# Kernel tuning notes

Measured on AMD Instinct MI355X. Metric: run time of the kernel, lower is better.

The kernel has to match this reference:

```python
import jax, jax.numpy as jnp
import numpy as np

N = 50000      # nodes
E = 800000     # edges
IN_DIM = 256
D = 32         # out_dim per head
H = 8          # num_heads
NEG_SLOPE = 0.01  # torch F.leaky_relu default


def setup_inputs() -> dict:
    key = jax.random.key(0)
    k1, k2, k3, k4, k5 = jax.random.split(key, 5)
    h = jax.random.normal(k1, (N, IN_DIM), dtype=jnp.float32)
    W = jax.random.normal(k2, (H, IN_DIM, D), dtype=jnp.float32) * 0.05
    attn_w = jax.random.normal(k3, (H, 2 * D), dtype=jnp.float32) * 0.05
    src = jax.random.randint(k4, (E,), 0, N, dtype=jnp.int64)
    dst = jax.random.randint(k5, (E,), 0, N, dtype=jnp.int64)
    return {"h": h, "W": W, "attn_w": attn_w, "src": src, "dst": dst}


def reference(h, W, attn_w, src, dst):
    # per-head linear projection: z[n,h,d]
    z = jnp.einsum('ni,hid->nhd', h, W)
    # attn_fc(concat(z_src, z_dst)) = z_src @ a_l + z_dst @ a_r
    a_l, a_r = attn_w[:, :D], attn_w[:, D:]
    el = jnp.einsum('nhd,hd->nh', z, a_l)  # [N,H]
    er = jnp.einsum('nhd,hd->nh', z, a_r)  # [N,H]
    e = jax.nn.leaky_relu(el[src] + er[dst], NEG_SLOPE)  # [E,H]
    # segment softmax over incoming edges of each destination node
    m = jax.ops.segment_max(e, dst, num_segments=N)      # [N,H]
    m = jnp.where(jnp.isfinite(m), m, 0.0)               # nodes w/ no in-edges
    num = jnp.exp(e - m[dst])                            # [E,H]
    den = jax.ops.segment_sum(num, dst, num_segments=N)  # [N,H]
    den_e = den[dst]
    alpha = num / jnp.where(den_e > 0, den_e, 1.0)       # [E,H]
    # weighted scatter-sum of source features
    msg = alpha[:, :, None] * z[src]                     # [E,H,D]
    hout = jax.ops.segment_sum(msg, dst, num_segments=N) # [N,H,D]
    # merge='cat': concat head outputs along feature dim
    return hout.reshape(N, H * D)
```

## Files before the change

### kernel.cpp

```cpp
#include <hip/hip_runtime.h>
#include <math.h>

#define NN 50000
#define EE 800000
#define INDIM 256
#define DD 32
#define HH 8
#define CC 256
#define NEG 0.01f
#define NREP 8
#define NSCAN 49
#define PREP_GRID 1024
#define PREP_STRIDE (PREP_GRID * 256)

typedef __attribute__((ext_vector_type(8))) short bf16x8;
typedef __attribute__((ext_vector_type(4))) float f32x4;

__device__ __forceinline__ unsigned short f32_to_bf16_rne(float f) {
  unsigned u = __float_as_uint(f);
  u += 0x7fffu + ((u >> 16) & 1u);
  return (unsigned short)(u >> 16);
}

__global__ __launch_bounds__(256) void k_prep(const unsigned* __restrict__ sraw,
                                              const unsigned* __restrict__ draw,
                                              int* __restrict__ counts8,
                                              unsigned short* __restrict__ s16,
                                              unsigned short* __restrict__ d16,
                                              unsigned short* __restrict__ slot16,
                                              const float* __restrict__ W,
                                              unsigned short* __restrict__ WbT) {
  __shared__ int sflag;
  if (threadIdx.x == 0) sflag = 0;
  __syncthreads();
  const int gt = blockIdx.x * 256 + threadIdx.x;
  unsigned v = 0;
#pragma unroll
  for (int i = 0; i < 4; ++i) {
    int e = (gt * 4 + i) % (EE / 2);
    v |= sraw[2 * e + 1] | draw[2 * e + 1];
  }
  if (v) atomicOr(&sflag, 1);
  __syncthreads();
  const int is32 = sflag;

  const int rep = blockIdx.x & (NREP - 1);
  int* __restrict__ mycounts = counts8 + rep * NN;

  for (int e = gt; e < EE; e += PREP_STRIDE) {
    int sv, dv;
    if (is32) {
      sv = ((const int*)sraw)[e];
      dv = ((const int*)draw)[e];
    } else {
      sv = (int)((const long long*)sraw)[e];
      dv = (int)((const long long*)draw)[e];
    }
    s16[e] = (unsigned short)sv;
    d16[e] = (unsigned short)dv;
    slot16[e] = (unsigned short)atomicAdd(&mycounts[dv], 1);
  }

  if (gt < INDIM * CC) {
    int n = gt >> 8, k = gt & 255;
    int hh = n >> 5, d = n & 31;
    WbT[gt] = f32_to_bf16_rne(W[(size_t)hh * 8192 + k * 32 + d]);
  }
}

__global__ __launch_bounds__(512) void k_gemm(const float* __restrict__ h,
                                              const unsigned short* __restrict__ WbT,
                                              const float* __restrict__ attn_w,
                                              signed char* __restrict__ z8,
                                              float* __restrict__ elsc,
                                              float* __restrict__ er) {
  __shared__ short sA[64 * 256];
  const int t = threadIdx.x;
  const int l = t & 63;
  const int w = t >> 6;
  const int row0 = blockIdx.x * 64;

#pragma unroll
  for (int i = 0; i < 4; ++i) {
    int q = i * 512 + t;
    int row = q >> 5, c = q & 31;
    int grow = row0 + row; if (grow >= NN) grow = NN - 1;
    const float* src = &h[(size_t)grow * 256 + c * 8];
    float4 f0 = *reinterpret_cast<const float4*>(src);
    float4 f1 = *reinterpret_cast<const float4*>(src + 4);
    bf16x8 vv;
    vv[0] = (short)f32_to_bf16_rne(f0.x); vv[1] = (short)f32_to_bf16_rne(f0.y);
    vv[2] = (short)f32_to_bf16_rne(f0.z); vv[3] = (short)f32_to_bf16_rne(f0.w);
    vv[4] = (short)f32_to_bf16_rne(f1.x); vv[5] = (short)f32_to_bf16_rne(f1.y);
    vv[6] = (short)f32_to_bf16_rne(f1.z); vv[7] = (short)f32_to_bf16_rne(f1.w);
    int sc = c ^ (row & 7);
    *reinterpret_cast<bf16x8*>(&sA[row * 256 + sc * 8]) = vv;
  }

  bf16x8 bf[2][8];
  {
    const int n = w * 32 + (l & 15);
    const int kb = (l >> 4) * 8;
#pragma unroll
    for (int c = 0; c < 2; ++c)
#pragma unroll
      for (int kk = 0; kk < 8; ++kk)
        bf[c][kk] = *reinterpret_cast<const bf16x8*>(
            &WbT[(size_t)(n + c * 16) * 256 + kk * 32 + kb]);
  }

  f32x4 acc[4][2];
#pragma unroll
  for (int m = 0; m < 4; ++m)
#pragma unroll
    for (int c = 0; c < 2; ++c) acc[m][c] = (f32x4){0.f, 0.f, 0.f, 0.f};

  __syncthreads();

#pragma unroll
  for (int kk = 0; kk < 8; ++kk) {
    bf16x8 af[4];
#pragma unroll
    for (int m = 0; m < 4; ++m) {
      int row = m * 16 + (l & 15);
      int chunk = kk * 4 + (l >> 4);
      int sc = chunk ^ (row & 7);
      af[m] = *reinterpret_cast<const bf16x8*>(&sA[row * 256 + sc * 8]);
    }
#pragma unroll
    for (int m = 0; m < 4; ++m)
#pragma unroll
      for (int c = 0; c < 2; ++c)
        acc[m][c] = __builtin_amdgcn_mfma_f32_16x16x32_bf16(bf[c][kk], af[m], acc[m][c], 0, 0, 0);
  }

  float alc[2][4], arc[2][4];
#pragma unroll
  for (int c = 0; c < 2; ++c)
#pragma unroll
    for (int r = 0; r < 4; ++r) {
      int d = c * 16 + ((l >> 4) << 2) + r;
      alc[c][r] = attn_w[w * 64 + d];
      arc[c][r] = attn_w[w * 64 + 32 + d];
    }

#pragma unroll
  for (int m = 0; m < 4; ++m) {
    int node = row0 + m * 16 + (l & 15);
    float pl = 0.f, pr = 0.f, pm = 0.f;
#pragma unroll
    for (int c = 0; c < 2; ++c)
#pragma unroll
      for (int r = 0; r < 4; ++r) {
        float a = acc[m][c][r];
        pl += a * alc[c][r];
        pr += a * arc[c][r];
        pm = fmaxf(pm, fabsf(a));
      }
    pl += __shfl_xor(pl, 16); pl += __shfl_xor(pl, 32);
    pr += __shfl_xor(pr, 16); pr += __shfl_xor(pr, 32);
    pm = fmaxf(pm, __shfl_xor(pm, 16)); pm = fmaxf(pm, __shfl_xor(pm, 32));
    const float rcp = (pm > 0.f) ? (127.f / pm) : 0.f;

    if (node < NN) {
#pragma unroll
      for (int c = 0; c < 2; ++c) {
        unsigned wq = 0;
#pragma unroll
        for (int r = 0; r < 4; ++r) {
          int q = __float2int_rn(acc[m][c][r] * rcp);
          wq |= ((unsigned)(q & 255)) << (8 * r);
        }
        *reinterpret_cast<unsigned*>(
            &z8[(size_t)node * CC + w * 32 + c * 16 + ((l >> 4) << 2)]) = wq;
      }
      if ((l >> 4) == 0) {
        elsc[(size_t)node * 16 + w] = pl;
        elsc[(size_t)node * 16 + 8 + w] = pm * (1.f / 127.f);
        er[(size_t)node * HH + w] = pr;
      }
    }
  }
}

__global__ __launch_bounds__(1024) void k_scan(const int* __restrict__ counts8,
                                               int* __restrict__ row_start,
                                               int* __restrict__ partial,
                                               unsigned char* __restrict__ offs8) {
  __shared__ int s[1024];
  const int tid = threadIdx.x;
  const int i = blockIdx.x * 1024 + tid;
  int deg = 0;
  if (i < NN) {
    unsigned pack0 = 0, pack1 = 0;
    int run = 0;
#pragma unroll
    for (int r = 0; r < NREP; ++r) {
      int c = counts8[r * NN + i];
      if (r < 4) pack0 |= (unsigned)run << (8 * r);
      else       pack1 |= (unsigned)run << (8 * (r - 4));
      run += c;
    }
    deg = run;
    uint2 pk; pk.x = pack0; pk.y = pack1;
    *reinterpret_cast<uint2*>(&offs8[(size_t)i * 8]) = pk;
  }
  s[tid] = deg;
  __syncthreads();
  for (int off = 1; off < 1024; off <<= 1) {
    int tv = (tid >= off) ? s[tid - off] : 0;
    __syncthreads();
    s[tid] += tv;
    __syncthreads();
  }
  if (i < NN) row_start[i] = s[tid] - deg;
  if (tid == 1023) partial[blockIdx.x] = s[1023];
}

__device__ __forceinline__ void block_base_scan(const int* __restrict__ partial,
                                                int* __restrict__ sbase) {
  if (threadIdx.x < 64) {
    int l = threadIdx.x;
    int x = (l < NSCAN) ? partial[l] : 0;
    int orig = x;
#pragma unroll
    for (int off = 1; off < 64; off <<= 1) {
      int y = __shfl_up(x, off);
      if (l >= off) x += y;
    }
    sbase[l] = x - orig;
  }
  __syncthreads();
}

__global__ __launch_bounds__(256) void k_scatter(const unsigned short* __restrict__ s16,
                                                 const unsigned short* __restrict__ d16,
                                                 const unsigned short* __restrict__ slot16,
                                                 const unsigned char* __restrict__ offs8,
                                                 const int* __restrict__ row_start,
                                                 const int* __restrict__ partial,
                                                 unsigned short* __restrict__ csr16) {
  __shared__ int sbase[64];
  block_base_scan(partial, sbase);
  int stride = gridDim.x * blockDim.x;
  for (int e = blockIdx.x * blockDim.x + threadIdx.x; e < EE; e += stride) {
    int dn = (int)d16[e];
    int rep = ((e & (PREP_STRIDE - 1)) >> 8) & (NREP - 1);
    int pos = row_start[dn] + sbase[dn >> 10] + (int)offs8[dn * 8 + rep] + (int)slot16[e];
    csr16[pos] = s16[e];
  }
}

#define AGG_WAVES 8192
__global__ __launch_bounds__(256) void k_agg(const signed char* __restrict__ z8,
                                             const float* __restrict__ elsc,
                                             const float* __restrict__ er,
                                             const int* __restrict__ row_start,
                                             const int* __restrict__ partial,
                                             const unsigned short* __restrict__ csr16,
                                             float* __restrict__ out) {
  __shared__ int sbase[64];
  block_base_scan(partial, sbase);

  const int gw = blockIdx.x * 4 + (threadIdx.x >> 6);
  const int l = threadIdx.x & 63;
  const int head = l >> 3;

  for (int n = gw; n < NN; n += AGG_WAVES) {
    const int beg = row_start[n] + sbase[n >> 10];
    const int end = (n == NN - 1) ? EE : (row_start[n + 1] + sbase[(n + 1) >> 10]);
    const float ern = er[(size_t)n * HH + head];

    float den = 0.f;
    float a0 = 0.f, a1 = 0.f, a2 = 0.f, a3 = 0.f;
#pragma unroll 4
    for (int p = beg; p < end; ++p) {
      int s = (int)csr16[p];
      float v = elsc[(size_t)s * 16 + head] + ern;
      v = (v > 0.f) ? v : v * NEG;
      float wgt = __expf(v);
      float sc = elsc[(size_t)s * 16 + 8 + head];
      unsigned wq = *reinterpret_cast<const unsigned*>(&z8[(size_t)s * CC + 4 * l]);
      den += wgt;
      float ws = wgt * sc;
      a0 += ws * (float)(int)(signed char)(wq & 255);
      a1 += ws * (float)(int)(signed char)((wq >> 8) & 255);
      a2 += ws * (float)(int)(signed char)((wq >> 16) & 255);
      a3 += ws * (float)(int)(signed char)(wq >> 24);
    }
    const float rd = (end > beg) ? (1.f / den) : 0.f;
    float4 o;
    o.x = a0 * rd; o.y = a1 * rd; o.z = a2 * rd; o.w = a3 * rd;
    *reinterpret_cast<float4*>(&out[(size_t)n * CC + 4 * l]) = o;
  }
}

extern "C" void kernel_launch(void* const* d_in, const int* in_sizes, int n_in,
                              void* d_out, int out_size, void* d_ws, size_t ws_size,
                              hipStream_t stream) {
  const float* h      = (const float*)d_in[0];
  const float* W      = (const float*)d_in[1];
  const float* attn_w = (const float*)d_in[2];
  const void*  src_raw = d_in[3];
  const void*  dst_raw = d_in[4];
  float* out = (float*)d_out;

  char* ws = (char*)d_ws;
  size_t off = 0;
  signed char* z8     = (signed char*)(ws + off); off += (size_t)NN * CC;
  unsigned short* WbT = (unsigned short*)(ws + off); off += (size_t)INDIM * CC * 2;
  float* elsc = (float*)(ws + off); off += (size_t)NN * 16 * 4;
  float* er   = (float*)(ws + off); off += (size_t)NN * HH * 4;
  int* counts8 = (int*)(ws + off); off += (size_t)NREP * NN * 4;
  int* row_start = (int*)(ws + off); off += (size_t)NN * 4;
  int* partial   = (int*)(ws + off); off += 256;
  unsigned char* offs8 = (unsigned char*)(ws + off); off += (size_t)NN * 8;
  unsigned short* s16    = (unsigned short*)(ws + off); off += (size_t)EE * 2;
  unsigned short* d16    = (unsigned short*)(ws + off); off += (size_t)EE * 2;
  unsigned short* slot16 = (unsigned short*)(ws + off); off += (size_t)EE * 2;
  unsigned short* csr16  = (unsigned short*)(ws + off); off += (size_t)EE * 2;

  hipMemsetAsync(counts8, 0, (size_t)NREP * NN * 4, stream);

  k_prep<<<PREP_GRID, 256, 0, stream>>>((const unsigned*)src_raw, (const unsigned*)dst_raw,
                                        counts8, s16, d16, slot16, W, WbT);

  k_gemm<<<(NN + 63) / 64, 512, 0, stream>>>(h, WbT, attn_w, z8, elsc, er);

  k_scan<<<NSCAN, 1024, 0, stream>>>(counts8, row_start, partial, offs8);

  k_scatter<<<2048, 256, 0, stream>>>(s16, d16, slot16, offs8, row_start, partial, csr16);

  k_agg<<<AGG_WAVES / 4, 256, 0, stream>>>(z8, elsc, er, row_start, partial, csr16, out);
}
```

Measured before the change: 146.6 us.

## Interleave two destination nodes per wave and pack el/scale as float2

The aggregation kernel now processes two destination nodes per wave, interleaving their edge loops over the common length so two independent gather chains are in flight. Tail loops finish the longer node. The per-node attention logit and quantization scale are stored interleaved as float2, so one 8-byte load replaces two scattered 4-byte loads. This raises memory-level parallelism for the latency-bound gathers, at the cost of more registers and possible imbalance between the paired nodes.

```diff
diff --git a/kernel.cpp b/kernel.cpp
--- a/kernel.cpp
+++ b/kernel.cpp
@@ -72,7 +72,7 @@
                                               const unsigned short* __restrict__ WbT,
                                               const float* __restrict__ attn_w,
                                               signed char* __restrict__ z8,
-                                              float* __restrict__ elsc,
+                                              float2* __restrict__ elsc,
                                               float* __restrict__ er) {
   __shared__ short sA[64 * 256];
   const int t = threadIdx.x;
@@ -175,8 +175,8 @@
             &z8[(size_t)node * CC + w * 32 + c * 16 + ((l >> 4) << 2)]) = wq;
       }
       if ((l >> 4) == 0) {
-        elsc[(size_t)node * 16 + w] = pl;
-        elsc[(size_t)node * 16 + 8 + w] = pm * (1.f / 127.f);
+        float2 e2; e2.x = pl; e2.y = pm * (1.f / 127.f);
+        elsc[(size_t)node * 8 + w] = e2;
         er[(size_t)node * HH + w] = pr;
       }
     }
@@ -252,8 +252,8 @@
 }
 
 #define AGG_WAVES 8192
-__global__ __launch_bounds__(256) void k_agg(const signed char* __restrict__ z8,
-                                             const float* __restrict__ elsc,
+__global__ __launch_bounds__(256) void k_agg(const unsigned* __restrict__ z8u,
+                                             const float2* __restrict__ elsc,
                                              const float* __restrict__ er,
                                              const int* __restrict__ row_start,
                                              const int* __restrict__ partial,
@@ -266,32 +266,75 @@
   const int l = threadIdx.x & 63;
   const int head = l >> 3;
 
-  for (int n = gw; n < NN; n += AGG_WAVES) {
-    const int beg = row_start[n] + sbase[n >> 10];
-    const int end = (n == NN - 1) ? EE : (row_start[n + 1] + sbase[(n + 1) >> 10]);
-    const float ern = er[(size_t)n * HH + head];
-
-    float den = 0.f;
-    float a0 = 0.f, a1 = 0.f, a2 = 0.f, a3 = 0.f;
-#pragma unroll 4
-    for (int p = beg; p < end; ++p) {
+  for (int n0 = gw * 2; n0 < NN; n0 += AGG_WAVES * 2) {
+    const int n1 = n0 + 1;
+    const int b0 = row_start[n0] + sbase[n0 >> 10];
+    const int e0 = row_start[n1] + sbase[n1 >> 10];
+    const int b1 = e0;
+    const int e1 = (n1 == NN - 1) ? EE : (row_start[n1 + 1] + sbase[(n1 + 1) >> 10]);
+    const float ern0 = er[(size_t)n0 * HH + head];
+    const float ern1 = er[(size_t)n1 * HH + head];
+
+    float den0 = 0.f, den1 = 0.f;
+    float a00 = 0.f, a01 = 0.f, a02 = 0.f, a03 = 0.f;
+    float a10 = 0.f, a11 = 0.f, a12 = 0.f, a13 = 0.f;
+
+    const int cd = min(e0 - b0, e1 - b1);
+#pragma unroll 2
+    for (int i = 0; i < cd; ++i) {
+      int sA_ = (int)csr16[b0 + i];
+      int sB_ = (int)csr16[b1 + i];
+      float2 eA = elsc[(size_t)sA_ * 8 + head];
+      float2 eB = elsc[(size_t)sB_ * 8 + head];
+      unsigned qA = z8u[(size_t)sA_ * 64 + l];
+      unsigned qB = z8u[(size_t)sB_ * 64 + l];
+      float vA = eA.x + ern0; vA = (vA > 0.f) ? vA : vA * NEG;
+      float vB = eB.x + ern1; vB = (vB > 0.f) ? vB : vB * NEG;
+      float wA = __expf(vA), wB = __expf(vB);
+      den0 += wA; den1 += wB;
+      float wsA = wA * eA.y, wsB = wB * eB.y;
+      a00 += wsA * (float)(int)(signed char)(qA & 255);
+      a01 += wsA * (float)(int)(signed char)((qA >> 8) & 255);
+      a02 += wsA * (float)(int)(signed char)((qA >> 16) & 255);
+      a03 += wsA * (float)(int)(signed char)(qA >> 24);
+      a10 += wsB * (float)(int)(signed char)(qB & 255);
+      a11 += wsB * (float)(int)(signed char)((qB >> 8) & 255);
+      a12 += wsB * (float)(int)(signed char)((qB >> 16) & 255);
+      a13 += wsB * (float)(int)(signed char)(qB >> 24);
+    }
+    for (int p = b0 + cd; p < e0; ++p) {
       int s = (int)csr16[p];
-      float v = elsc[(size_t)s * 16 + head] + ern;
-      v = (v > 0.f) ? v : v * NEG;
-      float wgt = __expf(v);
-      float sc = elsc[(size_t)s * 16 + 8 + head];
-      unsigned wq = *reinterpret_cast<const unsigned*>(&z8[(size_t)s * CC + 4 * l]);
-      den += wgt;
-      float ws = wgt * sc;
-      a0 += ws * (float)(int)(signed char)(wq & 255);
-      a1 += ws * (float)(int)(signed char)((wq >> 8) & 255);
-      a2 += ws * (float)(int)(signed char)((wq >> 16) & 255);
-      a3 += ws * (float)(int)(signed char)(wq >> 24);
-    }
-    const float rd = (end > beg) ? (1.f / den) : 0.f;
-    float4 o;
-    o.x = a0 * rd; o.y = a1 * rd; o.z = a2 * rd; o.w = a3 * rd;
-    *reinterpret_cast<float4*>(&out[(size_t)n * CC + 4 * l]) = o;
+      float2 eA = elsc[(size_t)s * 8 + head];
+      unsigned qA = z8u[(size_t)s * 64 + l];
+      float v = eA.x + ern0; v = (v > 0.f) ? v : v * NEG;
+      float w = __expf(v);
+      den0 += w;
+      float ws = w * eA.y;
+      a00 += ws * (float)(int)(signed char)(qA & 255);
+      a01 += ws * (float)(int)(signed char)((qA >> 8) & 255);
+      a02 += ws * (float)(int)(signed char)((qA >> 16) & 255);
+      a03 += ws * (float)(int)(signed char)(qA >> 24);
+    }
+    for (int p = b1 + cd; p < e1; ++p) {
+      int s = (int)csr16[p];
+      float2 eB = elsc[(size_t)s * 8 + head];
+      unsigned qB = z8u[(size_t)s * 64 + l];
+      float v = eB.x + ern1; v = (v > 0.f) ? v : v * NEG;
+      float w = __expf(v);
+      den1 += w;
+      float ws = w * eB.y;
+      a10 += ws * (float)(int)(signed char)(qB & 255);
+      a11 += ws * (float)(int)(signed char)((qB >> 8) & 255);
+      a12 += ws * (float)(int)(signed char)((qB >> 16) & 255);
+      a13 += ws * (float)(int)(signed char)(qB >> 24);
+    }
+
+    const float rd0 = (e0 > b0) ? (1.f / den0) : 0.f;
+    const float rd1 = (e1 > b1) ? (1.f / den1) : 0.f;
+    float4 o0; o0.x = a00 * rd0; o0.y = a01 * rd0; o0.z = a02 * rd0; o0.w = a03 * rd0;
+    float4 o1; o1.x = a10 * rd1; o1.y = a11 * rd1; o1.z = a12 * rd1; o1.w = a13 * rd1;
+    *reinterpret_cast<float4*>(&out[(size_t)n0 * CC + 4 * l]) = o0;
+    *reinterpret_cast<float4*>(&out[(size_t)n1 * CC + 4 * l]) = o1;
   }
 }
 
@@ -309,7 +352,7 @@
   size_t off = 0;
   signed char* z8     = (signed char*)(ws + off); off += (size_t)NN * CC;
   unsigned short* WbT = (unsigned short*)(ws + off); off += (size_t)INDIM * CC * 2;
-  float* elsc = (float*)(ws + off); off += (size_t)NN * 16 * 4;
+  float2* elsc = (float2*)(ws + off); off += (size_t)NN * 8 * 8;
   float* er   = (float*)(ws + off); off += (size_t)NN * HH * 4;
   int* counts8 = (int*)(ws + off); off += (size_t)NREP * NN * 4;
   int* row_start = (int*)(ws + off); off += (size_t)NN * 4;
@@ -331,5 +374,6 @@
 
   k_scatter<<<2048, 256, 0, stream>>>(s16, d16, slot16, offs8, row_start, partial, csr16);
 
-  k_agg<<<AGG_WAVES / 4, 256, 0, stream>>>(z8, elsc, er, row_start, partial, csr16, out);
-}
+  k_agg<<<AGG_WAVES / 4, 256, 0, stream>>>((const unsigned*)z8, elsc, er,
+                                           row_start, partial, csr16, out);
+}
```

After: 152.5 us. 4.0% more time.
